# Kernel tuning notes

Hardware: AMD Instinct MI355X
Metric: run time of the kernel (lower is better)

The kernel has to match this reference:

```python
import jax, jax.numpy as jnp
import numpy as np

# ---- constants derived exactly as in CQCCExtractor.__init__ ----
SR = 16000
FMIN = 32.7
N_BINS = 96
BINS_OCT = 24
N_CQCC = 20
HOP = 128
Q = 1.0 / (2.0 ** (1.0 / BINS_OCT) - 1.0)
MIN_WIN = max(16, int(Q * SR / FMIN))          # 16699
N_FFT = 1
while N_FFT < MIN_WIN * 2:
    N_FFT <<= 1                                # 65536
NUM_FREQ = N_FFT // 2 + 1                      # 32769


def _dct_mat():
    k = np.arange(N_CQCC)[:, None]
    n = np.arange(N_BINS)[None, :]
    return jnp.asarray(np.cos(np.pi * k * (2 * n + 1) / (2 * N_BINS)), dtype=jnp.float32)


def _delta(feat, N=2):
    # vectorized version of the per-frame python loop: d[t] = sum_n n*(f[min(t+n,T-1)] - f[max(t-n,0)]) / denom
    denom = 2 * sum(i * i for i in range(1, N + 1))
    T = feat.shape[0]
    p = jnp.concatenate([jnp.repeat(feat[:1], N, axis=0), feat, jnp.repeat(feat[-1:], N, axis=0)], axis=0)
    num = sum(n * (p[N + n:N + n + T] - p[N - n:N - n + T]) for n in range(1, N + 1))
    return num / denom


def setup_inputs() -> dict:
    key = jax.random.key(0)
    wav = jax.random.normal(key, (262144,), dtype=jnp.float32)
    return {"wav": wav}


def reference(wav) -> jnp.ndarray:
    # periodic hann window of length MIN_WIN, zero-padded (centered) to N_FFT like torch.stft
    w = 0.5 - 0.5 * jnp.cos(2.0 * jnp.pi * jnp.arange(MIN_WIN, dtype=jnp.float32) / MIN_WIN)
    left = (N_FFT - MIN_WIN) // 2
    win = jnp.zeros((N_FFT,), dtype=jnp.float32).at[left:left + MIN_WIN].set(w)

    # torch.stft(center=True, pad_mode='reflect')
    pad = N_FFT // 2
    x = jnp.pad(wav, pad, mode='reflect')
    n_frames = 1 + wav.shape[0] // HOP
    starts = jnp.arange(n_frames) * HOP
    frames = x[starts[:, None] + jnp.arange(N_FFT)[None, :]] * win      # [T, n_fft]
    spec = jnp.fft.rfft(frames, axis=-1)                                 # [T, F] complex64
    power = jnp.abs(spec) ** 2                                           # [T, F]

    # linear interpolation of STFT power at geometrically spaced CQT freqs
    cqt_freqs = FMIN * 2.0 ** (jnp.arange(N_BINS, dtype=jnp.float32) / BINS_OCT)
    idx_float = cqt_freqs / (SR / 2) * (NUM_FREQ - 1)
    idx_lo = jnp.clip(idx_float.astype(jnp.int32), 0, NUM_FREQ - 2)
    idx_hi = idx_lo + 1
    alpha = (idx_float - idx_lo.astype(jnp.float32))                     # [n_bins]
    cqt_power = (1.0 - alpha) * power[:, idx_lo] + alpha * power[:, idx_hi]  # [T, n_bins]

    log_cqt = jnp.log(jnp.maximum(cqt_power, 1e-8))
    cqcc = log_cqt @ _dct_mat().T                                        # [T, n_cqcc]
    # normalize over time (torch.std default is unbiased, ddof=1)
    cqcc = (cqcc - cqcc.mean(axis=0)) / (jnp.std(cqcc, axis=0, ddof=1) + 1e-8)

    d1 = _delta(cqcc)
    d2 = _delta(d1)
    return jnp.concatenate([cqcc, d1, d2], axis=-1)                      # [T, 3*n_cqcc]
```

## Files before the change

### kernel.cpp

```cpp
#include <hip/hip_runtime.h>
#include <math.h>

#define WAV_N     262144
#define HOP       128
#define MIN_WIN   16699
#define LEFT      24418
#define T_FRAMES  2049
#define N_BINS    96
#define N_CQCC    20
#define F_COMP    192
#define NF        576
#define NBLK      2179
#define NBP       2240
#define PARTLEN   59
#define FULLBLK   130
#define XS_VALID  278843
#define TWOPI     6.283185307179586f

#define BT   32
#define FTW  32
#define AST  34

#define WS_QFP  0
#define WS_SC   20643840
#define WS_CQ   23801856
#define WS_SUMS 23965776
#define SCP     2056

__device__ __forceinline__ void f_to_fi_sigma(int f, int& fi, int& sigma) {
    int plane = f / 192;
    int c = f - plane * 192;
    int bin = c >> 1, hi = c & 1;
    float e    = (float)bin / 24.0f;
    float fb   = 32.7f * exp2f(e);
    float idxf = fb / 8000.0f * 32768.0f;
    fi = (int)idxf + hi;
    sigma = (plane == 0) ? 0 : (plane == 1 ? 1 : -1);
}

__global__ __launch_bounds__(256) void k_chunk(const float* __restrict__ wav,
                                               float4* __restrict__ QFP) {
    __shared__ float A_lds[128 * AST];
    int tid = threadIdx.x;
    int b0 = blockIdx.x * BT;
    int f0 = blockIdx.y * FTW;

    {
        int sbase = 128 * b0;
        #pragma unroll
        for (int k = 0; k < 16; ++k) {
            int m = k * 256 + tid;
            int j = m & 127, bl = m >> 7;
            int s = sbase + m;
            float v = 0.0f;
            if (s < XS_VALID) {
                int w = s - 8350;
                if (w < 0) w = -w;
                if (w >= WAV_N) w = 2 * WAV_N - 2 - w;
                v = wav[w];
            }
            A_lds[j * AST + bl] = v;
        }
    }

    int f  = f0 + (tid & 31);
    int bg = tid >> 5;
    int bl0 = bg * 4;
    int bb = b0 + bl0;

    int fi, sg;
    f_to_fi_sigma(f, fi, sg);

    float Dr, Di;
    {
        float fr = (float)fi * (1.0f / 65536.0f) - (float)sg * (1.0f / (float)MIN_WIN);
        fr -= rintf(fr);
        float sn, cs; __sincosf(TWOPI * fr, &sn, &cs);
        Dr = cs; Di = -sn;
    }
    float Wr = 1.0f, Wi = 0.0f;

    float xr[4] = {0, 0, 0, 0}, xi[4] = {0, 0, 0, 0};
    float pr[4], pi[4];

    __syncthreads();

    #pragma unroll 4
    for (int j = 0; j < PARTLEN; ++j) {
        float2 a01 = *(const float2*)&A_lds[j * AST + bl0];
        float2 a23 = *(const float2*)&A_lds[j * AST + bl0 + 2];
        const float aa[4] = {a01.x, a01.y, a23.x, a23.y};
        #pragma unroll
        for (int i = 0; i < 4; ++i) {
            xr[i] = fmaf(aa[i], Wr, xr[i]);
            xi[i] = fmaf(aa[i], Wi, xi[i]);
        }
        float wr = Wr;
        Wr = wr * Dr - Wi * Di;
        Wi = wr * Di + Wi * Dr;
    }
    #pragma unroll
    for (int i = 0; i < 4; ++i) { pr[i] = xr[i]; pi[i] = xi[i]; }
    #pragma unroll 4
    for (int j = PARTLEN; j < 128; ++j) {
        float2 a01 = *(const float2*)&A_lds[j * AST + bl0];
        float2 a23 = *(const float2*)&A_lds[j * AST + bl0 + 2];
        const float aa[4] = {a01.x, a01.y, a23.x, a23.y};
        #pragma unroll
        for (int i = 0; i < 4; ++i) {
            xr[i] = fmaf(aa[i], Wr, xr[i]);
            xi[i] = fmaf(aa[i], Wi, xi[i]);
        }
        float wr = Wr;
        Wr = wr * Dr - Wi * Di;
        Wi = wr * Di + Wi * Dr;
    }

    float4* dst = QFP + (size_t)f * NBP + bb;
    #pragma unroll
    for (int i = 0; i < 4; ++i) {
        int b = bb + i;
        unsigned ph = ((unsigned)fi * (unsigned)(LEFT + 128 * b)) & 65535u;
        float frf = (float)ph * (1.0f / 65536.0f)
                  - (float)sg * (float)((128 * b) % MIN_WIN) * (1.0f / (float)MIN_WIN);
        frf -= rintf(frf);
        float sn, cs; __sincosf(TWOPI * frf, &sn, &cs);
        dst[i] = make_float4(xr[i] * cs + xi[i] * sn,
                             xi[i] * cs - xr[i] * sn,
                             pr[i] * cs + pi[i] * sn,
                             pi[i] * cs - pr[i] * sn);
    }
}

#define SEG 9
__global__ __launch_bounds__(256) void k_scan(const float4* __restrict__ QFP,
                                              float2* __restrict__ Sc,
                                              double* __restrict__ sums) {
    __shared__ float2 col[3 * NBLK];
    __shared__ double2 wsum[3][4];
    int tid = threadIdx.x;
    int c = blockIdx.x;
    if (c == 0 && tid < 40) sums[tid] = 0.0;

    const float2* base = (const float2*)QFP;
    #pragma unroll
    for (int p = 0; p < 3; ++p) {
        size_t foff = (size_t)(p * 192 + c) * NBP;
        #pragma unroll
        for (int k = 0; k < SEG; ++k) {
            int idx = k * 256 + tid;
            if (idx < NBLK) col[p * NBLK + idx] = base[2 * (foff + idx)];
        }
    }
    __syncthreads();

    int s0 = tid * SEG, s1 = min(s0 + SEG, NBLK);
    double sr[3] = {0, 0, 0}, si[3] = {0, 0, 0};
    #pragma unroll
    for (int p = 0; p < 3; ++p)
        for (int i = s0; i < s1; ++i) {
            sr[p] += col[p * NBLK + i].x;
            si[p] += col[p * NBLK + i].y;
        }
    double r[3], im[3];
    #pragma unroll
    for (int p = 0; p < 3; ++p) { r[p] = sr[p]; im[p] = si[p]; }
    #pragma unroll
    for (int off = 1; off < 64; off <<= 1) {
        #pragma unroll
        for (int p = 0; p < 3; ++p) {
            double prx = __shfl_up(r[p], off);
            double piy = __shfl_up(im[p], off);
            if ((tid & 63) >= off) { r[p] += prx; im[p] += piy; }
        }
    }
    if ((tid & 63) == 63) {
        #pragma unroll
        for (int p = 0; p < 3; ++p) wsum[p][tid >> 6] = make_double2(r[p], im[p]);
    }
    __syncthreads();
    int w = tid >> 6;
    double gr[3], gi[3];
    #pragma unroll
    for (int p = 0; p < 3; ++p) {
        double basr = 0.0, basi = 0.0;
        for (int ww = 0; ww < w; ++ww) { basr += wsum[p][ww].x; basi += wsum[p][ww].y; }
        gr[p] = basr + r[p] - sr[p];
        gi[p] = basi + im[p] - si[p];
    }
    for (int i = s0; i < s1; ++i) {
        #pragma unroll
        for (int p = 0; p < 3; ++p) {
            float2 old = col[p * NBLK + i];
            col[p * NBLK + i] = make_float2((float)gr[p], (float)gi[p]);
            gr[p] += old.x; gi[p] += old.y;
        }
    }
    __syncthreads();

    int fi_[3], sg_[3];
    #pragma unroll
    for (int p = 0; p < 3; ++p) f_to_fi_sigma(p * 192 + c, fi_[p], sg_[p]);
    #pragma unroll
    for (int k = 0; k < SEG; ++k) {
        int t = k * 256 + tid;
        if (t < T_FRAMES) {
            float accx = 0.0f, accy = 0.0f;
            #pragma unroll
            for (int p = 0; p < 3; ++p) {
                float2 g0 = col[p * NBLK + t];
                float2 g1 = col[p * NBLK + t + FULLBLK];
                float2 qp = base[2 * ((size_t)(p * 192 + c) * NBP + t + FULLBLK) + 1];
                float ur = g1.x - g0.x + qp.x;
                float ui = g1.y - g0.y + qp.y;
                unsigned ph = ((unsigned)fi_[p] * 128u * (unsigned)t) & 65535u;
                float frf = (float)ph * (1.0f / 65536.0f)
                          - (float)sg_[p] * (float)((128 * t) % MIN_WIN) * (1.0f / (float)MIN_WIN);
                frf -= rintf(frf);
                float sn, cs;
                __sincosf(TWOPI * frf, &sn, &cs);
                float vr = ur * cs - ui * sn;
                float vi = ur * sn + ui * cs;
                float wgt = (p == 0) ? 0.5f : -0.25f;
                accx = fmaf(wgt, vr, accx);
                accy = fmaf(wgt, vi, accy);
            }
            Sc[(size_t)c * SCP + t] = make_float2(accx, accy);
        }
    }
}

__global__ __launch_bounds__(256) void k_cqt(const float2* __restrict__ Sc,
                                             float* __restrict__ cq,
                                             double* __restrict__ sums) {
    __shared__ float dctm[N_CQCC * N_BINS];
    __shared__ float lg[8][N_BINS];
    __shared__ float cqv[8][N_CQCC];
    int tid = threadIdx.x;
    int tb = blockIdx.x * 8;
    for (int idx = tid; idx < N_CQCC * N_BINS; idx += 256) {
        int k = idx / N_BINS, b = idx - k * N_BINS;
        dctm[idx] = cosf((float)M_PI * (float)(k * (2 * b + 1)) / 192.0f);
    }
    int lt = tid >> 5, lane = tid & 31;
    int t = tb + lt;
    #pragma unroll
    for (int bb = 0; bb < 3; ++bb) {
        int b = lane + 32 * bb;
        float lv = 0.0f;
        if (t < T_FRAMES) {
            float2 lo = Sc[(size_t)(2 * b) * SCP + t];
            float2 hi = Sc[(size_t)(2 * b + 1) * SCP + t];
            float pl = lo.x * lo.x + lo.y * lo.y;
            float ph = hi.x * hi.x + hi.y * hi.y;
            float e    = (float)b / 24.0f;
            float fb   = 32.7f * exp2f(e);
            float idxf = fb / 8000.0f * 32768.0f;
            float alpha = idxf - (float)((int)idxf);
            float p = (1.0f - alpha) * pl + alpha * ph;
            lv = logf(fmaxf(p, 1e-8f));
        }
        lg[lt][b] = lv;
    }
    __syncthreads();
    if (tid < 8 * N_CQCC) {
        int lt2 = tid / N_CQCC, k = tid - lt2 * N_CQCC;
        int t2 = tb + lt2;
        float s = 0.0f;
        #pragma unroll 4
        for (int b = 0; b < N_BINS; ++b) s += dctm[k * N_BINS + b] * lg[lt2][b];
        cqv[lt2][k] = (t2 < T_FRAMES) ? s : 0.0f;
        if (t2 < T_FRAMES) cq[t2 * N_CQCC + k] = s;
    }
    __syncthreads();
    if (tid < N_CQCC) {
        double s1 = 0.0, s2 = 0.0;
        #pragma unroll
        for (int lt2 = 0; lt2 < 8; ++lt2) {
            if (tb + lt2 < T_FRAMES) {
                double v = (double)cqv[lt2][tid];
                s1 += v; s2 += v * v;
            }
        }
        atomicAdd(&sums[tid], s1);
        atomicAdd(&sums[N_CQCC + tid], s2);
    }
}

__device__ __forceinline__ int clampT(int v) {
    return v < 0 ? 0 : (v > T_FRAMES - 1 ? T_FRAMES - 1 : v);
}

__global__ void k_final(const float* __restrict__ cq, const double* __restrict__ sums,
                        float* __restrict__ out) {
    int gid = blockIdx.x * blockDim.x + threadIdx.x;
    if (gid >= T_FRAMES * N_CQCC) return;
    int t = gid / N_CQCC;
    int k = gid - t * N_CQCC;
    double S1 = sums[k], S2 = sums[N_CQCC + k];
    double md = S1 / (double)T_FRAMES;
    double var = (S2 - S1 * md) / (double)(T_FRAMES - 1);
    double sd = sqrt(var > 0.0 ? var : 0.0);
    float m = (float)md;
    float iv = (float)(1.0 / (sd + 1e-8));
    float cv[9];
    #pragma unroll
    for (int j = 0; j < 9; ++j)
        cv[j] = (cq[clampT(t + j - 4) * N_CQCC + k] - m) * iv;
    float dv[5];
    #pragma unroll
    for (int o = -2; o <= 2; ++o) {
        int p = clampT(t + o);
        int h1 = clampT(p + 1) - t, l1 = clampT(p - 1) - t;
        int h2 = clampT(p + 2) - t, l2 = clampT(p - 2) - t;
        dv[o + 2] = ((cv[h1 + 4] - cv[l1 + 4]) + 2.0f * (cv[h2 + 4] - cv[l2 + 4])) * 0.1f;
    }
    out[t * 60 + k]      = cv[4];
    out[t * 60 + 20 + k] = dv[2];
    out[t * 60 + 40 + k] = (dv[3] - dv[1] + 2.0f * (dv[4] - dv[0])) * 0.1f;
}

extern "C" void kernel_launch(void* const* d_in, const int* in_sizes, int n_in,
                              void* d_out, int out_size, void* d_ws, size_t ws_size,
                              hipStream_t stream) {
    const float* wav = (const float*)d_in[0];
    float* out = (float*)d_out;
    char* ws = (char*)d_ws;
    float4* QFP  = (float4*)(ws + WS_QFP);
    float2* Sc   = (float2*)(ws + WS_SC);
    float*  cq   = (float*)(ws + WS_CQ);
    double* sums = (double*)(ws + WS_SUMS);

    k_chunk<<<dim3(NBP / BT, NF / FTW), 256, 0, stream>>>(wav, QFP);
    k_scan<<<F_COMP, 256, 0, stream>>>(QFP, Sc, sums);
    k_cqt<<<(T_FRAMES + 7) / 8, 256, 0, stream>>>(Sc, cq, sums);
    k_final<<<(T_FRAMES * N_CQCC + 255) / 256, 256, 0, stream>>>(cq, sums, out);
}
```

Before: 108.2 us.

## Split scan per frequency plane and move plane combination into CQT kernel

The prefix-scan kernel now runs one 512-thread block per frequency row (576 blocks) instead of one 256-thread block handling three planes (192 blocks). This raises parallelism on a GPU with many CUs. Each block loads full float4 rows into LDS and reuses the .zw components instead of issuing a second strided global load. The weighted combination of the three planes moves into k_cqt, which now stages 16 frames per block through LDS. The cost is a larger intermediate buffer written and read from global memory, plus three gathered reads per element in k_cqt.

```diff
diff --git a/kernel.cpp b/kernel.cpp
--- a/kernel.cpp
+++ b/kernel.cpp
@@ -22,10 +22,10 @@
 #define AST  34
 
 #define WS_QFP  0
-#define WS_SC   20643840
-#define WS_CQ   23801856
-#define WS_SUMS 23965776
-#define SCP     2056
+#define WS_V    20643840
+#define WS_CQ   30117888
+#define WS_SUMS 30281808
+#define VTP     2056
 
 __device__ __forceinline__ void f_to_fi_sigma(int f, int& fi, int& sigma) {
     int plane = f / 192;
@@ -132,153 +132,126 @@
     }
 }
 
-#define SEG 9
-__global__ __launch_bounds__(256) void k_scan(const float4* __restrict__ QFP,
-                                              float2* __restrict__ Sc,
+#define SEG 5
+__global__ __launch_bounds__(512) void k_scan(const float4* __restrict__ QFP,
+                                              float2* __restrict__ V,
                                               double* __restrict__ sums) {
-    __shared__ float2 col[3 * NBLK];
-    __shared__ double2 wsum[3][4];
+    __shared__ float4 col[NBLK];
+    __shared__ double2 wsum[8];
     int tid = threadIdx.x;
-    int c = blockIdx.x;
-    if (c == 0 && tid < 40) sums[tid] = 0.0;
-
-    const float2* base = (const float2*)QFP;
-    #pragma unroll
-    for (int p = 0; p < 3; ++p) {
-        size_t foff = (size_t)(p * 192 + c) * NBP;
-        #pragma unroll
-        for (int k = 0; k < SEG; ++k) {
-            int idx = k * 256 + tid;
-            if (idx < NBLK) col[p * NBLK + idx] = base[2 * (foff + idx)];
-        }
+    int f = blockIdx.x;
+    if (f == 0 && tid < 40) sums[tid] = 0.0;
+
+    const float4* g = QFP + (size_t)f * NBP;
+    #pragma unroll
+    for (int k = 0; k < SEG; ++k) {
+        int idx = k * 512 + tid;
+        if (idx < NBLK) col[idx] = g[idx];
     }
     __syncthreads();
 
     int s0 = tid * SEG, s1 = min(s0 + SEG, NBLK);
-    double sr[3] = {0, 0, 0}, si[3] = {0, 0, 0};
-    #pragma unroll
-    for (int p = 0; p < 3; ++p)
-        for (int i = s0; i < s1; ++i) {
-            sr[p] += col[p * NBLK + i].x;
-            si[p] += col[p * NBLK + i].y;
-        }
-    double r[3], im[3];
-    #pragma unroll
-    for (int p = 0; p < 3; ++p) { r[p] = sr[p]; im[p] = si[p]; }
+    double sr = 0.0, si = 0.0;
+    for (int i = s0; i < s1; ++i) { sr += col[i].x; si += col[i].y; }
+    double r = sr, im = si;
     #pragma unroll
     for (int off = 1; off < 64; off <<= 1) {
-        #pragma unroll
-        for (int p = 0; p < 3; ++p) {
-            double prx = __shfl_up(r[p], off);
-            double piy = __shfl_up(im[p], off);
-            if ((tid & 63) >= off) { r[p] += prx; im[p] += piy; }
-        }
-    }
-    if ((tid & 63) == 63) {
-        #pragma unroll
-        for (int p = 0; p < 3; ++p) wsum[p][tid >> 6] = make_double2(r[p], im[p]);
-    }
-    __syncthreads();
+        double prx = __shfl_up(r, off);
+        double piy = __shfl_up(im, off);
+        if ((tid & 63) >= off) { r += prx; im += piy; }
+    }
+    if ((tid & 63) == 63) wsum[tid >> 6] = make_double2(r, im);
+    __syncthreads();
+    double basr = 0.0, basi = 0.0;
     int w = tid >> 6;
-    double gr[3], gi[3];
-    #pragma unroll
-    for (int p = 0; p < 3; ++p) {
-        double basr = 0.0, basi = 0.0;
-        for (int ww = 0; ww < w; ++ww) { basr += wsum[p][ww].x; basi += wsum[p][ww].y; }
-        gr[p] = basr + r[p] - sr[p];
-        gi[p] = basi + im[p] - si[p];
-    }
+    for (int ww = 0; ww < w; ++ww) { basr += wsum[ww].x; basi += wsum[ww].y; }
+    double gr = basr + r - sr, gi = basi + im - si;
     for (int i = s0; i < s1; ++i) {
-        #pragma unroll
-        for (int p = 0; p < 3; ++p) {
-            float2 old = col[p * NBLK + i];
-            col[p * NBLK + i] = make_float2((float)gr[p], (float)gi[p]);
-            gr[p] += old.x; gi[p] += old.y;
-        }
-    }
-    __syncthreads();
-
-    int fi_[3], sg_[3];
-    #pragma unroll
-    for (int p = 0; p < 3; ++p) f_to_fi_sigma(p * 192 + c, fi_[p], sg_[p]);
+        float qx = col[i].x, qy = col[i].y;
+        col[i].x = (float)gr; col[i].y = (float)gi;
+        gr += qx; gi += qy;
+    }
+    __syncthreads();
+
+    int fi_, sg_; f_to_fi_sigma(f, fi_, sg_);
+    float2* vrow = V + (size_t)f * VTP;
     #pragma unroll
     for (int k = 0; k < SEG; ++k) {
-        int t = k * 256 + tid;
+        int t = k * 512 + tid;
         if (t < T_FRAMES) {
-            float accx = 0.0f, accy = 0.0f;
-            #pragma unroll
-            for (int p = 0; p < 3; ++p) {
-                float2 g0 = col[p * NBLK + t];
-                float2 g1 = col[p * NBLK + t + FULLBLK];
-                float2 qp = base[2 * ((size_t)(p * 192 + c) * NBP + t + FULLBLK) + 1];
-                float ur = g1.x - g0.x + qp.x;
-                float ui = g1.y - g0.y + qp.y;
-                unsigned ph = ((unsigned)fi_[p] * 128u * (unsigned)t) & 65535u;
-                float frf = (float)ph * (1.0f / 65536.0f)
-                          - (float)sg_[p] * (float)((128 * t) % MIN_WIN) * (1.0f / (float)MIN_WIN);
-                frf -= rintf(frf);
-                float sn, cs;
-                __sincosf(TWOPI * frf, &sn, &cs);
-                float vr = ur * cs - ui * sn;
-                float vi = ur * sn + ui * cs;
-                float wgt = (p == 0) ? 0.5f : -0.25f;
-                accx = fmaf(wgt, vr, accx);
-                accy = fmaf(wgt, vi, accy);
-            }
-            Sc[(size_t)c * SCP + t] = make_float2(accx, accy);
-        }
-    }
-}
-
-__global__ __launch_bounds__(256) void k_cqt(const float2* __restrict__ Sc,
+            float4 ca = col[t];
+            float4 cb = col[t + FULLBLK];
+            float ur = cb.x - ca.x + cb.z;
+            float ui = cb.y - ca.y + cb.w;
+            unsigned ph = ((unsigned)fi_ * 128u * (unsigned)t) & 65535u;
+            float frf = (float)ph * (1.0f / 65536.0f)
+                      - (float)sg_ * (float)((128 * t) % MIN_WIN) * (1.0f / (float)MIN_WIN);
+            frf -= rintf(frf);
+            float sn, cs;
+            __sincosf(TWOPI * frf, &sn, &cs);
+            vrow[t] = make_float2(ur * cs - ui * sn, ur * sn + ui * cs);
+        }
+    }
+}
+
+#define TF16 16
+__global__ __launch_bounds__(256) void k_cqt(const float2* __restrict__ V,
                                              float* __restrict__ cq,
                                              double* __restrict__ sums) {
     __shared__ float dctm[N_CQCC * N_BINS];
-    __shared__ float lg[8][N_BINS];
-    __shared__ float cqv[8][N_CQCC];
+    __shared__ float2 sc[F_COMP * TF16];
+    __shared__ float lg[N_BINS * TF16];
+    __shared__ float cqv[N_CQCC * TF16];
     int tid = threadIdx.x;
-    int tb = blockIdx.x * 8;
+    int tb = blockIdx.x * TF16;
     for (int idx = tid; idx < N_CQCC * N_BINS; idx += 256) {
         int k = idx / N_BINS, b = idx - k * N_BINS;
         dctm[idx] = cosf((float)M_PI * (float)(k * (2 * b + 1)) / 192.0f);
     }
-    int lt = tid >> 5, lane = tid & 31;
-    int t = tb + lt;
-    #pragma unroll
-    for (int bb = 0; bb < 3; ++bb) {
-        int b = lane + 32 * bb;
-        float lv = 0.0f;
+    for (int idx = tid; idx < F_COMP * TF16; idx += 256) {
+        int c = idx >> 4, tl = idx & 15;
+        int t = tb + tl;
+        float2 v = make_float2(0.f, 0.f);
         if (t < T_FRAMES) {
-            float2 lo = Sc[(size_t)(2 * b) * SCP + t];
-            float2 hi = Sc[(size_t)(2 * b + 1) * SCP + t];
-            float pl = lo.x * lo.x + lo.y * lo.y;
-            float ph = hi.x * hi.x + hi.y * hi.y;
-            float e    = (float)b / 24.0f;
-            float fb   = 32.7f * exp2f(e);
-            float idxf = fb / 8000.0f * 32768.0f;
-            float alpha = idxf - (float)((int)idxf);
-            float p = (1.0f - alpha) * pl + alpha * ph;
-            lv = logf(fmaxf(p, 1e-8f));
-        }
-        lg[lt][b] = lv;
-    }
-    __syncthreads();
-    if (tid < 8 * N_CQCC) {
-        int lt2 = tid / N_CQCC, k = tid - lt2 * N_CQCC;
-        int t2 = tb + lt2;
+            float2 v0 = V[(size_t)c * VTP + t];
+            float2 v1 = V[(size_t)(192 + c) * VTP + t];
+            float2 v2 = V[(size_t)(384 + c) * VTP + t];
+            v = make_float2(0.5f * v0.x - 0.25f * (v1.x + v2.x),
+                            0.5f * v0.y - 0.25f * (v1.y + v2.y));
+        }
+        sc[idx] = v;
+    }
+    __syncthreads();
+    for (int idx = tid; idx < N_BINS * TF16; idx += 256) {
+        int b = idx >> 4, tl = idx & 15;
+        float2 lo = sc[(2 * b) * TF16 + tl];
+        float2 hi = sc[(2 * b + 1) * TF16 + tl];
+        float pl = lo.x * lo.x + lo.y * lo.y;
+        float ph = hi.x * hi.x + hi.y * hi.y;
+        float e    = (float)b / 24.0f;
+        float fb   = 32.7f * exp2f(e);
+        float idxf = fb / 8000.0f * 32768.0f;
+        float alpha = idxf - (float)((int)idxf);
+        float p = (1.0f - alpha) * pl + alpha * ph;
+        lg[idx] = logf(fmaxf(p, 1e-8f));
+    }
+    __syncthreads();
+    for (int idx = tid; idx < N_CQCC * TF16; idx += 256) {
+        int k = idx >> 4, tl = idx & 15;
+        int t = tb + tl;
         float s = 0.0f;
         #pragma unroll 4
-        for (int b = 0; b < N_BINS; ++b) s += dctm[k * N_BINS + b] * lg[lt2][b];
-        cqv[lt2][k] = (t2 < T_FRAMES) ? s : 0.0f;
-        if (t2 < T_FRAMES) cq[t2 * N_CQCC + k] = s;
+        for (int b = 0; b < N_BINS; ++b) s += dctm[k * N_BINS + b] * lg[b * TF16 + tl];
+        cqv[idx] = (t < T_FRAMES) ? s : 0.0f;
+        if (t < T_FRAMES) cq[t * N_CQCC + k] = s;
     }
     __syncthreads();
     if (tid < N_CQCC) {
         double s1 = 0.0, s2 = 0.0;
         #pragma unroll
-        for (int lt2 = 0; lt2 < 8; ++lt2) {
-            if (tb + lt2 < T_FRAMES) {
-                double v = (double)cqv[lt2][tid];
+        for (int tl = 0; tl < TF16; ++tl) {
+            if (tb + tl < T_FRAMES) {
+                double v = (double)cqv[tid * TF16 + tl];
                 s1 += v; s2 += v * v;
             }
         }
@@ -327,12 +300,12 @@
     float* out = (float*)d_out;
     char* ws = (char*)d_ws;
     float4* QFP  = (float4*)(ws + WS_QFP);
-    float2* Sc   = (float2*)(ws + WS_SC);
+    float2* V    = (float2*)(ws + WS_V);
     float*  cq   = (float*)(ws + WS_CQ);
     double* sums = (double*)(ws + WS_SUMS);
 
     k_chunk<<<dim3(NBP / BT, NF / FTW), 256, 0, stream>>>(wav, QFP);
-    k_scan<<<F_COMP, 256, 0, stream>>>(QFP, Sc, sums);
-    k_cqt<<<(T_FRAMES + 7) / 8, 256, 0, stream>>>(Sc, cq, sums);
+    k_scan<<<NF, 512, 0, stream>>>(QFP, V, sums);
+    k_cqt<<<(T_FRAMES + TF16 - 1) / TF16, 256, 0, stream>>>(V, cq, sums);
     k_final<<<(T_FRAMES * N_CQCC + 255) / 256, 256, 0, stream>>>(cq, sums, out);
 }
```

Result: no change. 106.8 us (median of 2 runs) (-1.3%).
